# Performance work log

Measured on AMD Instinct MI355X. Metric: run time of the kernel, lower is better.

Reference implementation:

```python
import jax, jax.numpy as jnp
import numpy as np

B, S, D, H = 2, 2048, 1024, 16
DK = D // H


def setup_inputs() -> dict:
    key = jax.random.key(0)
    ks = jax.random.split(key, 12)
    lim = 1.0 / np.sqrt(D)
    def lin(kw, kb):
        W = jax.random.uniform(kw, (D, D), jnp.float32, -lim, lim)
        b = jax.random.uniform(kb, (D,), jnp.float32, -lim, lim)
        return W, b
    Wq, bq = lin(ks[0], ks[1])
    Wk, bk = lin(ks[2], ks[3])
    Wv, bv = lin(ks[4], ks[5])
    Wo, bo = lin(ks[6], ks[7])
    Q = jax.random.normal(ks[8], (B, S, D), jnp.float32)
    K = jax.random.normal(ks[9], (B, S, D), jnp.float32)
    V = jax.random.normal(ks[10], (B, S, D), jnp.float32)
    # causal mask, broadcastable to (B, H, S, S)
    mask = jnp.broadcast_to(jnp.tril(jnp.ones((S, S), jnp.bool_))[None, None], (B, 1, S, S))
    return {"Q": Q, "K": K, "V": V, "mask": mask,
            "Wq": Wq, "bq": bq, "Wk": Wk, "bk": bk,
            "Wv": Wv, "bv": bv, "Wo": Wo, "bo": bo}


def reference(Q, K, V, mask, Wq, bq, Wk, bk, Wv, bv, Wo, bo):
    def split(x):  # (B,S,D) -> (B,H,S,DK)
        return x.reshape(B, S, H, DK).transpose(0, 2, 1, 3)
    q = split(Q @ Wq.T + bq)
    k = split(K @ Wk.T + bk)
    v = split(V @ Wv.T + bv)
    scores = jnp.einsum('bhqd,bhkd->bhqk', q, k) / jnp.sqrt(jnp.float32(DK))
    scores = jnp.where(mask, scores, jnp.float32(-1e9))
    probs = jax.nn.softmax(scores, axis=-1)
    out = jnp.einsum('bhqk,bhkd->bhqd', probs, v)  # (B,H,S,DK)
    out = out.transpose(0, 2, 1, 3).reshape(B, S, D)
    return out @ Wo.T + bo
```

## Files before the change

### kernel.cpp

```cpp
#include <hip/hip_runtime.h>

#define S_LEN 2048
#define D_DIM 1024
#define H_NUM 16
#define DK_DIM 64
#define BATCH 2
#define M_TOT (BATCH * S_LEN)
#define XSZ 4194304
#define WSZ 1048576
#define SCALE_LOG2 0.18033688f

typedef __bf16 bf16x8 __attribute__((ext_vector_type(8)));
typedef float f32x4 __attribute__((ext_vector_type(4)));
typedef unsigned short u16;

__device__ inline u16 f2bf(float f) {
  union { float f; unsigned u; } v; v.f = f;
  unsigned u = v.u;
  return (u16)((u + 0x7FFFu + ((u >> 16) & 1u)) >> 16);
}

typedef const __attribute__((address_space(1))) unsigned int gu32;
typedef __attribute__((address_space(3))) unsigned int lu32;
__device__ inline void glds16(const u16* g, u16* l) {
  __builtin_amdgcn_global_load_lds((gu32*)g, (lu32*)l, 16, 0, 0);
}

__global__ __launch_bounds__(256)
void convert_kernel(const float* __restrict__ Q, const float* __restrict__ K,
                    const float* __restrict__ V, const float* __restrict__ Wq,
                    const float* __restrict__ Wk, const float* __restrict__ Wv,
                    const float* __restrict__ Wo, u16* __restrict__ Xb,
                    u16* __restrict__ Wb) {
  const size_t e = ((size_t)blockIdx.x * 256 + threadIdx.x) * 8;
  const float* src;
  u16* dst;
  size_t off;
  if (e < 3ull * XSZ) {
    const int a = (int)(e >> 22);
    src = (a == 0) ? Q : (a == 1) ? K : V;
    off = e - ((size_t)a << 22);
    dst = Xb + e;
  } else {
    const size_t ew = e - 3ull * XSZ;
    const int a = (int)(ew >> 20);
    src = (a == 0) ? Wq : (a == 1) ? Wk : (a == 2) ? Wv : Wo;
    off = ew - ((size_t)a << 20);
    dst = Wb + ew;
  }
  const float4 v0 = *reinterpret_cast<const float4*>(&src[off]);
  const float4 v1 = *reinterpret_cast<const float4*>(&src[off + 4]);
  ushort4 w0, w1;
  w0.x = f2bf(v0.x); w0.y = f2bf(v0.y); w0.z = f2bf(v0.z); w0.w = f2bf(v0.w);
  w1.x = f2bf(v1.x); w1.y = f2bf(v1.y); w1.z = f2bf(v1.z); w1.w = f2bf(v1.w);
  *reinterpret_cast<ushort4*>(dst) = w0;
  *reinterpret_cast<ushort4*>(dst + 4) = w1;
}

__global__ __launch_bounds__(256)
void proj_kernel(const u16* __restrict__ Qb, const u16* __restrict__ Kb,
                 const u16* __restrict__ Vb, const u16* __restrict__ Wqb,
                 const u16* __restrict__ Wkb, const u16* __restrict__ Wvb,
                 const float* __restrict__ bq, const float* __restrict__ bk,
                 const float* __restrict__ bv, u16* __restrict__ qh,
                 u16* __restrict__ kh, u16* __restrict__ vt) {
  const int z = blockIdx.z;
  const u16* A  = (z == 0) ? Qb : (z == 1) ? Kb : Vb;
  const u16* Bw = (z == 0) ? Wqb : (z == 1) ? Wkb : Wvb;
  const float* bias = (z == 0) ? bq : (z == 1) ? bk : bv;
  u16* out = (z == 0) ? qh : (z == 1) ? kh : vt;
  const float oscale = (z == 0) ? SCALE_LOG2 : 1.0f;

  __shared__ __align__(16) u16 Asm[2][128 * 64];
  __shared__ __align__(16) u16 Bsm[2][128 * 64];

  const int tid = threadIdx.x;
  const int m0 = blockIdx.x * 128, n0 = blockIdx.y * 128;
  const int wid = tid >> 6, lane = tid & 63;
  const int col = lane & 15, quad = lane >> 4;
  const int wm = (wid >> 1) * 64, wn = (wid & 1) * 64;

  const int lr = lane >> 3;
  const int lc = (lane & 7) ^ lr;
  const u16* gA = A + (size_t)(m0 + 32 * wid + lr) * D_DIM + lc * 8;
  const u16* gB = Bw + (size_t)(n0 + 32 * wid + lr) * D_DIM + lc * 8;

  f32x4 acc[4][4];
  const f32x4 zero4 = {0.f, 0.f, 0.f, 0.f};
  for (int i = 0; i < 4; i++)
    for (int j = 0; j < 4; j++) acc[i][j] = zero4;

  for (int j = 0; j < 4; j++) {
    glds16(gA + (size_t)j * 8 * D_DIM, &Asm[0][(32 * wid + 8 * j) * 64]);
    glds16(gB + (size_t)j * 8 * D_DIM, &Bsm[0][(32 * wid + 8 * j) * 64]);
  }

  for (int ks = 0; ks < 16; ks++) {
    const int b = ks & 1;
    __syncthreads();

    if (ks + 1 < 16) {
      const int k1 = (ks + 1) * 64;
      for (int j = 0; j < 4; j++) {
        glds16(gA + (size_t)j * 8 * D_DIM + k1,
               &Asm[b ^ 1][(32 * wid + 8 * j) * 64]);
        glds16(gB + (size_t)j * 8 * D_DIM + k1,
               &Bsm[b ^ 1][(32 * wid + 8 * j) * 64]);
      }
    }

    bf16x8 af[4][2], bfm[4][2];
    for (int i = 0; i < 4; i++) {
      const int row = wm + i * 16 + col;
      const int r7 = row & 7;
      af[i][0] = *reinterpret_cast<const bf16x8*>(&Asm[b][row * 64 + ((quad ^ r7) * 8)]);
      af[i][1] = *reinterpret_cast<const bf16x8*>(&Asm[b][row * 64 + (((quad + 4) ^ r7) * 8)]);
    }
    for (int j = 0; j < 4; j++) {
      const int row = wn + j * 16 + col;
      const int r7 = row & 7;
      bfm[j][0] = *reinterpret_cast<const bf16x8*>(&Bsm[b][row * 64 + ((quad ^ r7) * 8)]);
      bfm[j][1] = *reinterpret_cast<const bf16x8*>(&Bsm[b][row * 64 + (((quad + 4) ^ r7) * 8)]);
    }
    if (z == 2) {
      for (int h = 0; h < 2; h++)
        for (int i = 0; i < 4; i++)
          for (int j = 0; j < 4; j++)
            acc[i][j] = __builtin_amdgcn_mfma_f32_16x16x32_bf16(
                af[i][h], bfm[j][h], acc[i][j], 0, 0, 0);
    } else {
      for (int h = 0; h < 2; h++)
        for (int i = 0; i < 4; i++)
          for (int j = 0; j < 4; j++)
            acc[i][j] = __builtin_amdgcn_mfma_f32_16x16x32_bf16(
                bfm[j][h], af[i][h], acc[i][j], 0, 0, 0);
    }
  }

  if (z != 2) {
    float4 b4[4];
    for (int j = 0; j < 4; j++)
      b4[j] = *reinterpret_cast<const float4*>(&bias[n0 + wn + j * 16 + quad * 4]);
    for (int i = 0; i < 4; i++) {
      const int token = m0 + wm + i * 16 + col;
      const int b = token >> 11, s = token & (S_LEN - 1);
      for (int j = 0; j < 4; j++) {
        const int gnb = n0 + wn + j * 16 + quad * 4;
        const int h = gnb >> 6, dk = gnb & 63;
        ushort4 w;
        w.x = f2bf((acc[i][j][0] + b4[j].x) * oscale);
        w.y = f2bf((acc[i][j][1] + b4[j].y) * oscale);
        w.z = f2bf((acc[i][j][2] + b4[j].z) * oscale);
        w.w = f2bf((acc[i][j][3] + b4[j].w) * oscale);
        *reinterpret_cast<ushort4*>(
            &out[((size_t)(b * H_NUM + h) * S_LEN + s) * DK_DIM + dk]) = w;
      }
    }
  } else {
    float bb[4];
    for (int j = 0; j < 4; j++) bb[j] = bias[n0 + wn + j * 16 + col];
    for (int i = 0; i < 4; i++) {
      const int token0 = m0 + wm + i * 16 + quad * 4;
      const int b = token0 >> 11, s0 = token0 & (S_LEN - 1);
      for (int j = 0; j < 4; j++) {
        const int gn = n0 + wn + j * 16 + col;
        const int h = gn >> 6, dk = gn & 63;
        ushort4 w;
        w.x = f2bf(acc[i][j][0] + bb[j]);
        w.y = f2bf(acc[i][j][1] + bb[j]);
        w.z = f2bf(acc[i][j][2] + bb[j]);
        w.w = f2bf(acc[i][j][3] + bb[j]);
        *reinterpret_cast<ushort4*>(
            &out[((size_t)(b * H_NUM + h) * DK_DIM + dk) * S_LEN + s0]) = w;
      }
    }
  }
}

__global__ __launch_bounds__(256)
void attn_kernel(const u16* __restrict__ qh, const u16* __restrict__ kh,
                 const u16* __restrict__ vt, u16* __restrict__ ctx) {
  __shared__ __align__(16) u16 Ksm[2][64 * 64];
  __shared__ __align__(16) u16 Vsm[2][64 * 64];
  __shared__ __align__(16) u16 Psm[4][16][72];

  const int tid  = threadIdx.x;
  const int flat = blockIdx.x;
  const int qb   = 31 - (flat >> 5);
  const int bh   = flat & 31;
  const int wid  = tid >> 6;
  const int lane = tid & 63;
  const int col  = lane & 15;
  const int quad = lane >> 4;
  const int r7   = col & 7;

  const int lr = lane >> 3;
  const int lc = (lane & 7) ^ lr;
  const u16* kbase = kh + ((size_t)bh * S_LEN + 16 * wid + lr) * DK_DIM + lc * 8;
  const u16* vbase = vt + ((size_t)bh * DK_DIM + 16 * wid + lr) * S_LEN + lc * 8;

  const f32x4 zero4 = {0.f, 0.f, 0.f, 0.f};
  const int b_ = bh >> 4, h_ = bh & 15;

  const int nt = qb + 1;
  const int qrow_w = qb * 64 + wid * 16;
  const int qg = qrow_w + col;

  bf16x8 qB[2];
  {
    const u16* qp = &qh[((size_t)bh * S_LEN + qg) * DK_DIM + quad * 8];
    qB[0] = *reinterpret_cast<const bf16x8*>(qp);
    qB[1] = *reinterpret_cast<const bf16x8*>(qp + 32);
  }

  glds16(kbase, &Ksm[0][(16 * wid) * 64]);
  glds16(kbase + 8 * DK_DIM, &Ksm[0][(16 * wid + 8) * 64]);
  glds16(vbase, &Vsm[0][(16 * wid) * 64]);
  glds16(vbase + (size_t)8 * S_LEN, &Vsm[0][(16 * wid + 8) * 64]);

  float l_ = 0.f;
  f32x4 o[4];
  for (int dm = 0; dm < 4; dm++) o[dm] = zero4;

  for (int tt = 0; tt < nt; tt++) {
    const int b = tt & 1;
    __syncthreads();

    if (tt + 1 < nt) {
      const int nkv = (tt + 1) * 64;
      u16* kd = &Ksm[b ^ 1][(16 * wid) * 64];
      u16* vd = &Vsm[b ^ 1][(16 * wid) * 64];
      glds16(kbase + (size_t)nkv * DK_DIM, kd);
      glds16(kbase + (size_t)(nkv + 8) * DK_DIM, kd + 8 * 64);
      glds16(vbase + nkv, vd);
      glds16(vbase + (size_t)8 * S_LEN + nkv, vd + 8 * 64);
    }

    const int kv0 = tt * 64;
    f32x4 s[4];
    __builtin_amdgcn_s_setprio(1);
    for (int nc = 0; nc < 4; nc++) {
      const int row = nc * 16 + col;
      const bf16x8 kA0 = *reinterpret_cast<const bf16x8*>(
          &Ksm[b][row * 64 + ((quad ^ r7) * 8)]);
      const bf16x8 kA1 = *reinterpret_cast<const bf16x8*>(
          &Ksm[b][row * 64 + (((quad + 4) ^ r7) * 8)]);
      f32x4 acc = zero4;
      acc = __builtin_amdgcn_mfma_f32_16x16x32_bf16(kA0, qB[0], acc, 0, 0, 0);
      acc = __builtin_amdgcn_mfma_f32_16x16x32_bf16(kA1, qB[1], acc, 0, 0, 0);
      s[nc] = acc;
    }
    __builtin_amdgcn_s_setprio(0);

    const bool domask = (kv0 + 63 > qrow_w);
    for (int nc = 0; nc < 4; nc++) {
      const int kvb = kv0 + nc * 16 + quad * 4;
      float p[4];
      for (int r = 0; r < 4; r++) {
        float e = __builtin_amdgcn_exp2f(s[nc][r]);
        if (domask && (kvb + r > qg)) e = 0.f;
        p[r] = e;
      }
      unsigned u0 = __float_as_uint(p[0]), u1 = __float_as_uint(p[1]);
      unsigned u2 = __float_as_uint(p[2]), u3 = __float_as_uint(p[3]);
      l_ += __uint_as_float(u0 & 0xffff0000u);
      l_ += __uint_as_float(u1 & 0xffff0000u);
      l_ += __uint_as_float(u2 & 0xffff0000u);
      l_ += __uint_as_float(u3 & 0xffff0000u);
      uint2 pw;
      pw.x = __builtin_amdgcn_perm(u1, u0, 0x07060302);
      pw.y = __builtin_amdgcn_perm(u3, u2, 0x07060302);
      *reinterpret_cast<uint2*>(&Psm[wid][col][nc * 16 + quad * 4]) = pw;
    }

    asm volatile("s_waitcnt lgkmcnt(0)" ::: "memory");

    bf16x8 pB[2];
    pB[0] = *reinterpret_cast<const bf16x8*>(&Psm[wid][col][quad * 8]);
    pB[1] = *reinterpret_cast<const bf16x8*>(&Psm[wid][col][32 + quad * 8]);
    __builtin_amdgcn_s_setprio(1);
    for (int dm = 0; dm < 4; dm++) {
      const int row = dm * 16 + col;
      const bf16x8 vA0 = *reinterpret_cast<const bf16x8*>(
          &Vsm[b][row * 64 + ((quad ^ r7) * 8)]);
      const bf16x8 vA1 = *reinterpret_cast<const bf16x8*>(
          &Vsm[b][row * 64 + (((quad + 4) ^ r7) * 8)]);
      o[dm] = __builtin_amdgcn_mfma_f32_16x16x32_bf16(vA0, pB[0], o[dm], 0, 0, 0);
      o[dm] = __builtin_amdgcn_mfma_f32_16x16x32_bf16(vA1, pB[1], o[dm], 0, 0, 0);
    }
    __builtin_amdgcn_s_setprio(0);
  }

  float rs = l_;
  rs += __shfl_xor(rs, 16);
  rs += __shfl_xor(rs, 32);
  const float inv = 1.0f / rs;
  for (int dm = 0; dm < 4; dm++) {
    ushort4 w;
    w.x = f2bf(o[dm][0] * inv);
    w.y = f2bf(o[dm][1] * inv);
    w.z = f2bf(o[dm][2] * inv);
    w.w = f2bf(o[dm][3] * inv);
    *reinterpret_cast<ushort4*>(
        &ctx[((size_t)b_ * S_LEN + qg) * D_DIM + h_ * DK_DIM + dm * 16 +
             quad * 4]) = w;
  }
}

__global__ __launch_bounds__(256)
void outproj_kernel(const u16* __restrict__ ctx, const u16* __restrict__ Wob,
                    const float* __restrict__ bo, float* __restrict__ out) {
  __shared__ __align__(16) u16 Asm[2][64 * 64];
  __shared__ __align__(16) u16 Bsm[2][128 * 64];

  const int tid = threadIdx.x;
  const int m0 = blockIdx.x * 64, n0 = blockIdx.y * 128;
  const int wid = tid >> 6, lane = tid & 63;
  const int col = lane & 15, quad = lane >> 4;

  const int lr = lane >> 3;
  const int lc = (lane & 7) ^ lr;
  const u16* gA = ctx + (size_t)(m0 + 16 * wid + lr) * D_DIM + lc * 8;
  const u16* gB = Wob + (size_t)(n0 + 32 * wid + lr) * D_DIM + lc * 8;

  f32x4 acc[4][2];
  const f32x4 zero4 = {0.f, 0.f, 0.f, 0.f};
  for (int i = 0; i < 4; i++)
    for (int j = 0; j < 2; j++) acc[i][j] = zero4;

  for (int j = 0; j < 2; j++)
    glds16(gA + (size_t)j * 8 * D_DIM, &Asm[0][(16 * wid + 8 * j) * 64]);
  for (int j = 0; j < 4; j++)
    glds16(gB + (size_t)j * 8 * D_DIM, &Bsm[0][(32 * wid + 8 * j) * 64]);

  for (int ks = 0; ks < 16; ks++) {
    const int b = ks & 1;
    __syncthreads();

    if (ks + 1 < 16) {
      const int k1 = (ks + 1) * 64;
      for (int j = 0; j < 2; j++)
        glds16(gA + (size_t)j * 8 * D_DIM + k1,
               &Asm[b ^ 1][(16 * wid + 8 * j) * 64]);
      for (int j = 0; j < 4; j++)
        glds16(gB + (size_t)j * 8 * D_DIM + k1,
               &Bsm[b ^ 1][(32 * wid + 8 * j) * 64]);
    }

    bf16x8 af[4][2], bfm[2][2];
    for (int i = 0; i < 4; i++) {
      const int row = i * 16 + col;
      const int r7 = row & 7;
      af[i][0] = *reinterpret_cast<const bf16x8*>(&Asm[b][row * 64 + ((quad ^ r7) * 8)]);
      af[i][1] = *reinterpret_cast<const bf16x8*>(&Asm[b][row * 64 + (((quad + 4) ^ r7) * 8)]);
    }
    for (int j = 0; j < 2; j++) {
      const int row = 32 * wid + j * 16 + col;
      const int r7 = row & 7;
      bfm[j][0] = *reinterpret_cast<const bf16x8*>(&Bsm[b][row * 64 + ((quad ^ r7) * 8)]);
      bfm[j][1] = *reinterpret_cast<const bf16x8*>(&Bsm[b][row * 64 + (((quad + 4) ^ r7) * 8)]);
    }
    for (int h = 0; h < 2; h++)
      for (int i = 0; i < 4; i++)
        for (int j = 0; j < 2; j++)
          acc[i][j] = __builtin_amdgcn_mfma_f32_16x16x32_bf16(
              bfm[j][h], af[i][h], acc[i][j], 0, 0, 0);
  }

  float4 b4[2];
  for (int j = 0; j < 2; j++)
    b4[j] = *reinterpret_cast<const float4*>(
        &bo[n0 + 32 * wid + j * 16 + quad * 4]);
  for (int i = 0; i < 4; i++) {
    const int token = m0 + i * 16 + col;
    for (int j = 0; j < 2; j++) {
      const int gnb = n0 + 32 * wid + j * 16 + quad * 4;
      float4 v;
      v.x = acc[i][j][0] + b4[j].x;
      v.y = acc[i][j][1] + b4[j].y;
      v.z = acc[i][j][2] + b4[j].z;
      v.w = acc[i][j][3] + b4[j].w;
      *reinterpret_cast<float4*>(&out[(size_t)token * D_DIM + gnb]) = v;
    }
  }
}

extern "C" void kernel_launch(void* const* d_in, const int* in_sizes, int n_in,
                              void* d_out, int out_size, void* d_ws,
                              size_t ws_size, hipStream_t stream) {
  const float* Q  = (const float*)d_in[0];
  const float* K  = (const float*)d_in[1];
  const float* V  = (const float*)d_in[2];
  const float* Wq = (const float*)d_in[4];
  const float* bq = (const float*)d_in[5];
  const float* Wk = (const float*)d_in[6];
  const float* bk = (const float*)d_in[7];
  const float* Wv = (const float*)d_in[8];
  const float* bv = (const float*)d_in[9];
  const float* Wo = (const float*)d_in[10];
  const float* bo = (const float*)d_in[11];
  float* out = (float*)d_out;

  u16* qh  = (u16*)d_ws;
  u16* kh  = qh + XSZ;
  u16* vt  = kh + XSZ;
  u16* Qb  = vt + XSZ;
  u16* ctx = Qb;
  u16* Kb  = Qb + XSZ;
  u16* Vb  = Kb + XSZ;
  u16* Wqb = Vb + XSZ;
  u16* Wkb = Wqb + WSZ;
  u16* Wvb = Wkb + WSZ;
  u16* Wob = Wvb + WSZ;

  convert_kernel<<<(3 * XSZ + 4 * WSZ) / (256 * 8), 256, 0, stream>>>(
      Q, K, V, Wq, Wk, Wv, Wo, Qb, Wqb);

  proj_kernel<<<dim3(M_TOT / 128, D_DIM / 128, 3), 256, 0, stream>>>(
      Qb, Kb, Vb, Wqb, Wkb, Wvb, bq, bk, bv, qh, kh, vt);

  attn_kernel<<<dim3(1024), 256, 0, stream>>>(qh, kh, vt, ctx);

  outproj_kernel<<<dim3(M_TOT / 64, D_DIM / 128), 256, 0, stream>>>(ctx, Wob,
                                                                    bo, out);
}
```

Baseline: 238.6 us.

## Swizzle block order for XCD locality, single-buffer proj LDS, widen convert stores

Remaps the flat block index in the projection and output-projection kernels so that blocks landing on the same XCD (round-robin by 8) work on neighbouring tiles, improving L2 reuse of shared A/B panels. The projection kernel also drops its LDS double buffering in favour of a single buffer with load-then-sync per k-step, which halves shared memory (possibly raising occupancy) but loses the copy/compute overlap. The convert kernel now writes eight bf16 values with one 16-byte store instead of two 8-byte stores.

```diff
diff --git a/kernel.cpp b/kernel.cpp
--- a/kernel.cpp
+++ b/kernel.cpp
@@ -13,6 +13,7 @@
 typedef __bf16 bf16x8 __attribute__((ext_vector_type(8)));
 typedef float f32x4 __attribute__((ext_vector_type(4)));
 typedef unsigned short u16;
+typedef unsigned short u16x8 __attribute__((ext_vector_type(8)));
 
 __device__ inline u16 f2bf(float f) {
   union { float f; unsigned u; } v; v.f = f;
@@ -50,11 +51,10 @@
   }
   const float4 v0 = *reinterpret_cast<const float4*>(&src[off]);
   const float4 v1 = *reinterpret_cast<const float4*>(&src[off + 4]);
-  ushort4 w0, w1;
-  w0.x = f2bf(v0.x); w0.y = f2bf(v0.y); w0.z = f2bf(v0.z); w0.w = f2bf(v0.w);
-  w1.x = f2bf(v1.x); w1.y = f2bf(v1.y); w1.z = f2bf(v1.z); w1.w = f2bf(v1.w);
-  *reinterpret_cast<ushort4*>(dst) = w0;
-  *reinterpret_cast<ushort4*>(dst + 4) = w1;
+  u16x8 w;
+  w[0] = f2bf(v0.x); w[1] = f2bf(v0.y); w[2] = f2bf(v0.z); w[3] = f2bf(v0.w);
+  w[4] = f2bf(v1.x); w[5] = f2bf(v1.y); w[6] = f2bf(v1.z); w[7] = f2bf(v1.w);
+  *reinterpret_cast<u16x8*>(dst) = w;
 }
 
 __global__ __launch_bounds__(256)
@@ -64,18 +64,22 @@
                  const float* __restrict__ bq, const float* __restrict__ bk,
                  const float* __restrict__ bv, u16* __restrict__ qh,
                  u16* __restrict__ kh, u16* __restrict__ vt) {
-  const int z = blockIdx.z;
+  const int f = blockIdx.x + 32 * blockIdx.y + 256 * blockIdx.z;
+  const int swz = (f & 7) * 96 + (f >> 3);
+  const int z = swz >> 8;
+  const int bx = swz & 31, by = (swz >> 5) & 7;
+
   const u16* A  = (z == 0) ? Qb : (z == 1) ? Kb : Vb;
   const u16* Bw = (z == 0) ? Wqb : (z == 1) ? Wkb : Wvb;
   const float* bias = (z == 0) ? bq : (z == 1) ? bk : bv;
   u16* out = (z == 0) ? qh : (z == 1) ? kh : vt;
   const float oscale = (z == 0) ? SCALE_LOG2 : 1.0f;
 
-  __shared__ __align__(16) u16 Asm[2][128 * 64];
-  __shared__ __align__(16) u16 Bsm[2][128 * 64];
+  __shared__ __align__(16) u16 Asm[128 * 64];
+  __shared__ __align__(16) u16 Bsm[128 * 64];
 
   const int tid = threadIdx.x;
-  const int m0 = blockIdx.x * 128, n0 = blockIdx.y * 128;
+  const int m0 = bx * 128, n0 = by * 128;
   const int wid = tid >> 6, lane = tid & 63;
   const int col = lane & 15, quad = lane >> 4;
   const int wm = (wid >> 1) * 64, wn = (wid & 1) * 64;
@@ -90,37 +94,26 @@
   for (int i = 0; i < 4; i++)
     for (int j = 0; j < 4; j++) acc[i][j] = zero4;
 
-  for (int j = 0; j < 4; j++) {
-    glds16(gA + (size_t)j * 8 * D_DIM, &Asm[0][(32 * wid + 8 * j) * 64]);
-    glds16(gB + (size_t)j * 8 * D_DIM, &Bsm[0][(32 * wid + 8 * j) * 64]);
-  }
-
-  for (int ks = 0; ks < 16; ks++) {
-    const int b = ks & 1;
+  for (int k0 = 0; k0 < D_DIM; k0 += 64) {
     __syncthreads();
-
-    if (ks + 1 < 16) {
-      const int k1 = (ks + 1) * 64;
-      for (int j = 0; j < 4; j++) {
-        glds16(gA + (size_t)j * 8 * D_DIM + k1,
-               &Asm[b ^ 1][(32 * wid + 8 * j) * 64]);
-        glds16(gB + (size_t)j * 8 * D_DIM + k1,
-               &Bsm[b ^ 1][(32 * wid + 8 * j) * 64]);
-      }
-    }
+    for (int j = 0; j < 4; j++) {
+      glds16(gA + (size_t)j * 8 * D_DIM + k0, &Asm[(32 * wid + 8 * j) * 64]);
+      glds16(gB + (size_t)j * 8 * D_DIM + k0, &Bsm[(32 * wid + 8 * j) * 64]);
+    }
+    __syncthreads();
 
     bf16x8 af[4][2], bfm[4][2];
     for (int i = 0; i < 4; i++) {
       const int row = wm + i * 16 + col;
       const int r7 = row & 7;
-      af[i][0] = *reinterpret_cast<const bf16x8*>(&Asm[b][row * 64 + ((quad ^ r7) * 8)]);
-      af[i][1] = *reinterpret_cast<const bf16x8*>(&Asm[b][row * 64 + (((quad + 4) ^ r7) * 8)]);
+      af[i][0] = *reinterpret_cast<const bf16x8*>(&Asm[row * 64 + ((quad ^ r7) * 8)]);
+      af[i][1] = *reinterpret_cast<const bf16x8*>(&Asm[row * 64 + (((quad + 4) ^ r7) * 8)]);
     }
     for (int j = 0; j < 4; j++) {
       const int row = wn + j * 16 + col;
       const int r7 = row & 7;
-      bfm[j][0] = *reinterpret_cast<const bf16x8*>(&Bsm[b][row * 64 + ((quad ^ r7) * 8)]);
-      bfm[j][1] = *reinterpret_cast<const bf16x8*>(&Bsm[b][row * 64 + (((quad + 4) ^ r7) * 8)]);
+      bfm[j][0] = *reinterpret_cast<const bf16x8*>(&Bsm[row * 64 + ((quad ^ r7) * 8)]);
+      bfm[j][1] = *reinterpret_cast<const bf16x8*>(&Bsm[row * 64 + (((quad + 4) ^ r7) * 8)]);
     }
     if (z == 2) {
       for (int h = 0; h < 2; h++)
@@ -313,8 +306,11 @@
   __shared__ __align__(16) u16 Asm[2][64 * 64];
   __shared__ __align__(16) u16 Bsm[2][128 * 64];
 
+  const int f = blockIdx.x + 64 * blockIdx.y;
+  const int swz = (f & 7) * 64 + (f >> 3);
+  const int m0 = (swz & 63) * 64, n0 = (swz >> 6) * 128;
+
   const int tid = threadIdx.x;
-  const int m0 = blockIdx.x * 64, n0 = blockIdx.y * 128;
   const int wid = tid >> 6, lane = tid & 63;
   const int col = lane & 15, quad = lane >> 4;
 
```

Result: slower. 260.5 us (+9.2%).
